# Kernel tuning notes

Hardware: AMD Instinct MI355X
Metric: run time of the kernel (lower is better)

Reference implementation:

```python
import jax, jax.numpy as jnp
import numpy as np

B, S, D = 4, 2048, 2048
H, KVH = 16, 8
HD = D // H          # 128
N_REP = H // KVH     # 2


def _rope(t, cos, sin):
    # t: [B,S,h,HD]; cos/sin: [S, HD//2]
    tr = t.reshape(*t.shape[:-1], HD // 2, 2)
    t0, t1 = tr[..., 0], tr[..., 1]
    c = cos[None, :, None, :]
    s = sin[None, :, None, :]
    o0 = t0 * c - t1 * s
    o1 = t0 * s + t1 * c
    return jnp.stack([o0, o1], axis=-1).reshape(t.shape)


def setup_inputs() -> dict:
    key = jax.random.key(0)
    ks = jax.random.split(key, 7)
    x = jax.random.normal(ks[0], (B, S, D), dtype=jnp.float32)
    wq = jax.random.normal(ks[1], (D, H * HD), dtype=jnp.float32) * 0.02
    wk = jax.random.normal(ks[2], (D, KVH * HD), dtype=jnp.float32) * 0.02
    wv = jax.random.normal(ks[3], (D, KVH * HD), dtype=jnp.float32) * 0.02
    wo = jax.random.normal(ks[4], (H * HD, D), dtype=jnp.float32) * 0.02
    # rotary angles as in precompute_pos_cis: theta=1e6-style base 10000
    freqs = 1.0 / (10000.0 ** (jnp.arange(0, HD, 2, dtype=jnp.float32) / HD))
    ang = jnp.outer(jnp.arange(S, dtype=jnp.float32), freqs)  # [S, HD//2]
    return {"x": x, "wq": wq, "wk": wk, "wv": wv, "wo": wo,
            "pos_cos": jnp.cos(ang), "pos_sin": jnp.sin(ang)}


def reference(x, wq, wk, wv, wo, pos_cos, pos_sin):
    q = (x @ wq).reshape(B, S, H, HD)
    k = (x @ wk).reshape(B, S, KVH, HD)
    v = (x @ wv).reshape(B, S, KVH, HD)
    q = _rope(q, pos_cos, pos_sin)
    k = _rope(k, pos_cos, pos_sin)
    # GQA repeat_kv: [B,S,KVH,HD] -> [B,S,H,HD]
    k = jnp.repeat(k, N_REP, axis=2)
    v = jnp.repeat(v, N_REP, axis=2)
    scale = 1.0 / jnp.sqrt(jnp.float32(HD))
    scores = jnp.einsum('bqhd,bkhd->bhqk', q, k) * scale
    causal = jnp.tril(jnp.ones((S, S), dtype=bool))
    scores = jnp.where(causal[None, None], scores, jnp.float32(-jnp.inf))
    attn = jax.nn.softmax(scores, axis=-1)
    out = jnp.einsum('bhqk,bkhd->bqhd', attn, v).reshape(B, S, H * HD)
    return out @ wo
```

## Files before the change

kernel.cpp:

```cpp
#include <hip/hip_runtime.h>
#include <stdint.h>

#define SEQ   2048
#define DIM   2048
#define NH    16
#define NKVH  8
#define HDIM  128
#define MTOT  8192
#define LOG2E 1.44269504088896340736f

typedef short bf16x8 __attribute__((ext_vector_type(8)));
typedef float f32x4  __attribute__((ext_vector_type(4)));
typedef unsigned short us4 __attribute__((ext_vector_type(4)));

#define MFMA(a, b, c) __builtin_amdgcn_mfma_f32_16x16x32_bf16((a), (b), (c), 0, 0, 0)

__device__ inline unsigned short f2bf(float f) {
    unsigned u = __builtin_bit_cast(unsigned, f);
    u = (u + 0x7FFFu + ((u >> 16) & 1u)) >> 16;
    return (unsigned short)u;
}

__device__ inline void stage16(const void* g, void* l) {
    __builtin_amdgcn_global_load_lds(
        (const __attribute__((address_space(1))) void*)g,
        (__attribute__((address_space(3))) void*)l,
        16, 0, 0);
}

__global__ void conv_x(const float* __restrict__ x, unsigned short* __restrict__ xb) {
    long i = ((long)blockIdx.x * 256 + threadIdx.x) * 4;
    float4 v = *(const float4*)(x + i);
    us4 o = { f2bf(v.x), f2bf(v.y), f2bf(v.z), f2bf(v.w) };
    *(us4*)(xb + i) = o;
}

__global__ void transpose_w(const float* __restrict__ in, unsigned short* __restrict__ out,
                            int N, int row_off) {
    __shared__ float t[32][33];
    int tx = threadIdx.x, ty = threadIdx.y;
    int n0 = blockIdx.x * 32, k0 = blockIdx.y * 32;
    for (int i = 0; i < 4; i++)
        t[ty + i * 8][tx] = in[(long)(k0 + ty + i * 8) * N + n0 + tx];
    __syncthreads();
    for (int i = 0; i < 4; i++)
        out[(long)(row_off + n0 + ty + i * 8) * 2048 + k0 + tx] = f2bf(t[tx][ty + i * 8]);
}

__global__ void transpose_v(const unsigned short* __restrict__ v, unsigned short* __restrict__ vt) {
    __shared__ unsigned short t[32][33];
    int tx = threadIdx.x, ty = threadIdx.y;
    int d0 = blockIdx.x * 32, s0 = blockIdx.y * 32, bk = blockIdx.z;
    const unsigned short* vin = v + (long)bk * SEQ * HDIM;
    unsigned short* vo = vt + (long)bk * HDIM * SEQ;
    for (int i = 0; i < 4; i++)
        t[ty + i * 8][tx] = vin[(long)(s0 + ty + i * 8) * HDIM + d0 + tx];
    __syncthreads();
    for (int i = 0; i < 4; i++)
        vo[(long)(d0 + ty + i * 8) * SEQ + s0 + tx] = t[tx][ty + i * 8];
}

__launch_bounds__(256, 2)
__global__ void qkv_gemm(const unsigned short* __restrict__ xb,
                         const unsigned short* __restrict__ wt,
                         const float* __restrict__ pcos, const float* __restrict__ psin,
                         unsigned short* __restrict__ qb, unsigned short* __restrict__ kbuf,
                         unsigned short* __restrict__ vbuf) {
    constexpr int K = DIM;
    __shared__ __align__(16) unsigned short As[128 * 64];
    __shared__ __align__(16) unsigned short Bs[128 * 64];
    const int tid = threadIdx.x;
    const int m0 = blockIdx.y * 128;
    const int n0 = blockIdx.x * 128;
    const int w = tid >> 6, lane = tid & 63, qq = lane >> 4, ln = lane & 15;
    const int wm = w >> 1, wn = w & 1;

    f32x4 acc[4][4] = {};

    const int arow = tid >> 3;
    const int aswz = ((tid & 7) ^ (arow & 7)) * 8;
    const unsigned short* ag = xb + (long)(m0 + arow) * K + aswz;
    const unsigned short* bg = wt + (long)(n0 + arow) * K + aswz;
    unsigned short* al = As + tid * 8;
    unsigned short* bl = Bs + tid * 8;

    for (int kk = 0; kk < K; kk += 64) {
        __syncthreads();
        stage16(ag + kk,          al);
        stage16(ag + kk + 32 * K, al + 2048);
        stage16(ag + kk + 64 * K, al + 4096);
        stage16(ag + kk + 96 * K, al + 6144);
        stage16(bg + kk,          bl);
        stage16(bg + kk + 32 * K, bl + 2048);
        stage16(bg + kk + 64 * K, bl + 4096);
        stage16(bg + kk + 96 * K, bl + 6144);
        __syncthreads();
        bf16x8 a[2][4], b[2][4];
        for (int ks = 0; ks < 2; ks++) {
            for (int mt = 0; mt < 4; mt++)
                a[ks][mt] = *(const bf16x8*)&As[(wm * 64 + mt * 16 + ln) * 64 + (((ks * 4 + qq) ^ (ln & 7)) * 8)];
            for (int nt = 0; nt < 4; nt++)
                b[ks][nt] = *(const bf16x8*)&Bs[(wn * 64 + nt * 16 + ln) * 64 + (((ks * 4 + qq) ^ (ln & 7)) * 8)];
        }
        for (int ks = 0; ks < 2; ks++)
            for (int mt = 0; mt < 4; mt++)
                for (int nt = 0; nt < 4; nt++)
                    acc[mt][nt] = MFMA(b[ks][nt], a[ks][mt], acc[mt][nt]);
    }

    const bool isv = (n0 >= 3072);
    for (int mt = 0; mt < 4; mt++) {
        int m = m0 + wm * 64 + mt * 16 + ln;
        int b_ = m >> 11, s = m & (SEQ - 1);
        const float* crow = pcos + s * 64;
        const float* srow = psin + s * 64;
        for (int nt = 0; nt < 4; nt++) {
            int n = n0 + wn * 64 + nt * 16 + qq * 4;
            int d = n & (HDIM - 1);
            f32x4 v = acc[mt][nt];
            float o0, o1, o2, o3;
            if (!isv) {
                int i = d >> 1;
                float2 cc = *(const float2*)(crow + i);
                float2 ss = *(const float2*)(srow + i);
                o0 = v[0] * cc.x - v[1] * ss.x;
                o1 = v[0] * ss.x + v[1] * cc.x;
                o2 = v[2] * cc.y - v[3] * ss.y;
                o3 = v[2] * ss.y + v[3] * cc.y;
            } else {
                o0 = v[0]; o1 = v[1]; o2 = v[2]; o3 = v[3];
            }
            us4 pu = { f2bf(o0), f2bf(o1), f2bf(o2), f2bf(o3) };
            if (n < 2048) {
                int hh = n >> 7;
                *(us4*)&qb[((long)(b_ * NH + hh) * SEQ + s) * HDIM + d] = pu;
            } else if (n < 3072) {
                int kvh = (n - 2048) >> 7;
                *(us4*)&kbuf[((long)(b_ * NKVH + kvh) * SEQ + s) * HDIM + d] = pu;
            } else {
                int kvh = (n - 3072) >> 7;
                *(us4*)&vbuf[((long)(b_ * NKVH + kvh) * SEQ + s) * HDIM + d] = pu;
            }
        }
    }
}

__launch_bounds__(256, 2)
__global__ void flash(const unsigned short* __restrict__ qb,
                      const unsigned short* __restrict__ kb,
                      const unsigned short* __restrict__ vtb,
                      unsigned short* __restrict__ aout) {
    __shared__ __align__(16) unsigned short KV[32768];
    const int tid = threadIdx.x;
    const int w = tid >> 6, lane = tid & 63, qq = lane >> 4, ln = lane & 15;
    unsigned short* Pseg = KV + w * 4096;

    int f = blockIdx.x + (blockIdx.y << 3) + (blockIdx.z << 7);
    int xcd = f & 7, j = f >> 3;
    int bkv = xcd + 8 * (j & 3);
    int b = bkv >> 3, kv = bkv & 7;
    int rem = j >> 2;
    int h = kv * 2 + (rem & 1);
    int qpair = rem >> 1;

    const unsigned short* qbase = qb + (long)(b * NH + h) * SEQ * HDIM;
    const unsigned short* kbase = kb + (long)(b * NKVH + kv) * SEQ * HDIM;
    const unsigned short* vbase = vtb + (long)(b * NKVH + kv) * HDIM * SEQ;
    const float SCL2 = 0.088388347648318447f * LOG2E;

    const int srow = tid >> 4;
    const int sswz = (tid & 15) ^ srow;

    for (int phase = 0; phase < 2; phase++) {
        const int qt = (phase == 0) ? qpair : 15 - qpair;
        const int q0 = qt * 128 + w * 32;

        bf16x8 qf[2][4];
        for (int nt = 0; nt < 2; nt++)
            for (int ks = 0; ks < 4; ks++)
                qf[nt][ks] = *(const bf16x8*)&qbase[(long)(q0 + nt * 16 + ln) * HDIM + ks * 32 + qq * 8];

        float m[2] = { -3e38f, -3e38f }, l[2] = { 0.f, 0.f };
        f32x4 oacc[8][2] = {};

        #pragma unroll 1
        for (int kt = 0; kt <= qt; kt++) {
            const int k0 = kt * 128;

            __syncthreads();
            char* kl = (char*)KV;
            #pragma unroll
            for (int r = 0; r < 8; r++) {
                int key = r * 16 + srow;
                stage16(kbase + (long)(k0 + key) * HDIM + sswz * 8, kl + r * 4096 + tid * 16);
            }
            #pragma unroll
            for (int r = 0; r < 8; r++) {
                int hd = r * 16 + srow;
                stage16(vbase + (long)hd * SEQ + k0 + sswz * 8, kl + 32768 + r * 4096 + tid * 16);
            }
            __syncthreads();

            f32x4 sacc[8][2] = {};
            #pragma unroll
            for (int mt = 0; mt < 8; mt++) {
                const unsigned short* kr = &KV[(mt * 16 + ln) * 128];
                bf16x8 kf0 = *(const bf16x8*)&kr[((0 + qq) ^ ln) * 8];
                bf16x8 kf1 = *(const bf16x8*)&kr[((4 + qq) ^ ln) * 8];
                bf16x8 kf2 = *(const bf16x8*)&kr[((8 + qq) ^ ln) * 8];
                bf16x8 kf3 = *(const bf16x8*)&kr[((12 + qq) ^ ln) * 8];
                sacc[mt][0] = MFMA(kf0, qf[0][0], sacc[mt][0]);
                sacc[mt][1] = MFMA(kf0, qf[1][0], sacc[mt][1]);
                sacc[mt][0] = MFMA(kf1, qf[0][1], sacc[mt][0]);
                sacc[mt][1] = MFMA(kf1, qf[1][1], sacc[mt][1]);
                sacc[mt][0] = MFMA(kf2, qf[0][2], sacc[mt][0]);
                sacc[mt][1] = MFMA(kf2, qf[1][2], sacc[mt][1]);
                sacc[mt][0] = MFMA(kf3, qf[0][3], sacc[mt][0]);
                sacc[mt][1] = MFMA(kf3, qf[1][3], sacc[mt][1]);
            }

            __syncthreads();

            const bool diag = (kt == qt);
            #pragma unroll
            for (int nt = 0; nt < 2; nt++) {
                const int q = q0 + nt * 16 + ln;
                float mx = m[nt];
                #pragma unroll
                for (int mt = 0; mt < 8; mt++)
                    #pragma unroll
                    for (int r = 0; r < 4; r++) {
                        float v = sacc[mt][nt][r];
                        if (diag && (k0 + mt * 16 + qq * 4 + r > q)) v = -3e38f;
                        sacc[mt][nt][r] = v;
                        mx = fmaxf(mx, v);
                    }
                mx = fmaxf(mx, __shfl_xor(mx, 16));
                mx = fmaxf(mx, __shfl_xor(mx, 32));
                float alpha = exp2f((m[nt] - mx) * SCL2);
                m[nt] = mx;
                float rs = 0.f;
                #pragma unroll
                for (int mt = 0; mt < 8; mt++) {
                    float p0 = exp2f((sacc[mt][nt][0] - mx) * SCL2);
                    float p1 = exp2f((sacc[mt][nt][1] - mx) * SCL2);
                    float p2 = exp2f((sacc[mt][nt][2] - mx) * SCL2);
                    float p3 = exp2f((sacc[mt][nt][3] - mx) * SCL2);
                    rs += (p0 + p1) + (p2 + p3);
                    us4 pu = { f2bf(p0), f2bf(p1), f2bf(p2), f2bf(p3) };
                    *(us4*)&Pseg[(nt * 16 + ln) * 128 + ((mt * 2 + (qq >> 1)) ^ ln) * 8 + (qq & 1) * 4] = pu;
                }
                rs += __shfl_xor(rs, 16);
                rs += __shfl_xor(rs, 32);
                l[nt] = l[nt] * alpha + rs;
                #pragma unroll
                for (int mt = 0; mt < 8; mt++)
                    #pragma unroll
                    for (int r = 0; r < 4; r++)
                        oacc[mt][nt][r] *= alpha;
            }

            bf16x8 pf[4][2];
            #pragma unroll
            for (int ks = 0; ks < 4; ks++)
                #pragma unroll
                for (int nt = 0; nt < 2; nt++)
                    pf[ks][nt] = *(const bf16x8*)&Pseg[(nt * 16 + ln) * 128 + ((ks * 4 + qq) ^ ln) * 8];
            #pragma unroll
            for (int mt = 0; mt < 8; mt++) {
                const unsigned short* vr = &KV[16384 + (mt * 16 + ln) * 128];
                bf16x8 vf0 = *(const bf16x8*)&vr[((0 + qq) ^ ln) * 8];
                bf16x8 vf1 = *(const bf16x8*)&vr[((4 + qq) ^ ln) * 8];
                bf16x8 vf2 = *(const bf16x8*)&vr[((8 + qq) ^ ln) * 8];
                bf16x8 vf3 = *(const bf16x8*)&vr[((12 + qq) ^ ln) * 8];
                oacc[mt][0] = MFMA(vf0, pf[0][0], oacc[mt][0]);
                oacc[mt][1] = MFMA(vf0, pf[0][1], oacc[mt][1]);
                oacc[mt][0] = MFMA(vf1, pf[1][0], oacc[mt][0]);
                oacc[mt][1] = MFMA(vf1, pf[1][1], oacc[mt][1]);
                oacc[mt][0] = MFMA(vf2, pf[2][0], oacc[mt][0]);
                oacc[mt][1] = MFMA(vf2, pf[2][1], oacc[mt][1]);
                oacc[mt][0] = MFMA(vf3, pf[3][0], oacc[mt][0]);
                oacc[mt][1] = MFMA(vf3, pf[3][1], oacc[mt][1]);
            }
        }

        #pragma unroll
        for (int nt = 0; nt < 2; nt++) {
            const int q = q0 + nt * 16 + ln;
            float inv = 1.f / l[nt];
            unsigned short* ao = aout + ((long)b * SEQ + q) * DIM + h * HDIM;
            #pragma unroll
            for (int mt = 0; mt < 8; mt++) {
                us4 o = { f2bf(oacc[mt][nt][0] * inv), f2bf(oacc[mt][nt][1] * inv),
                          f2bf(oacc[mt][nt][2] * inv), f2bf(oacc[mt][nt][3] * inv) };
                *(us4*)&ao[mt * 16 + qq * 4] = o;
            }
        }
    }
}

__launch_bounds__(256, 2)
__global__ void out_gemm(const unsigned short* __restrict__ ab,
                         const unsigned short* __restrict__ wt,
                         float* __restrict__ out) {
    constexpr int K = DIM;
    __shared__ __align__(16) unsigned short As[128 * 64];
    __shared__ __align__(16) unsigned short Bs[128 * 64];
    const int tid = threadIdx.x;
    const int m0 = blockIdx.y * 128;
    const int n0 = blockIdx.x * 128;
    const int w = tid >> 6, lane = tid & 63, qq = lane >> 4, ln = lane & 15;
    const int wm = w >> 1, wn = w & 1;

    f32x4 acc[4][4] = {};

    const int arow = tid >> 3;
    const int aswz = ((tid & 7) ^ (arow & 7)) * 8;
    const unsigned short* ag = ab + (long)(m0 + arow) * K + aswz;
    const unsigned short* bg = wt + (long)(n0 + arow) * K + aswz;
    unsigned short* al = As + tid * 8;
    unsigned short* bl = Bs + tid * 8;

    for (int kk = 0; kk < K; kk += 64) {
        __syncthreads();
        stage16(ag + kk,          al);
        stage16(ag + kk + 32 * K, al + 2048);
        stage16(ag + kk + 64 * K, al + 4096);
        stage16(ag + kk + 96 * K, al + 6144);
        stage16(bg + kk,          bl);
        stage16(bg + kk + 32 * K, bl + 2048);
        stage16(bg + kk + 64 * K, bl + 4096);
        stage16(bg + kk + 96 * K, bl + 6144);
        __syncthreads();
        bf16x8 a[2][4], b[2][4];
        for (int ks = 0; ks < 2; ks++) {
            for (int mt = 0; mt < 4; mt++)
                a[ks][mt] = *(const bf16x8*)&As[(wm * 64 + mt * 16 + ln) * 64 + (((ks * 4 + qq) ^ (ln & 7)) * 8)];
            for (int nt = 0; nt < 4; nt++)
                b[ks][nt] = *(const bf16x8*)&Bs[(wn * 64 + nt * 16 + ln) * 64 + (((ks * 4 + qq) ^ (ln & 7)) * 8)];
        }
        for (int ks = 0; ks < 2; ks++)
            for (int mt = 0; mt < 4; mt++)
                for (int nt = 0; nt < 4; nt++)
                    acc[mt][nt] = MFMA(a[ks][mt], b[ks][nt], acc[mt][nt]);
    }

    for (int mt = 0; mt < 4; mt++)
        for (int nt = 0; nt < 4; nt++) {
            int n = n0 + wn * 64 + nt * 16 + ln;
            for (int r = 0; r < 4; r++) {
                int m = m0 + wm * 64 + mt * 16 + qq * 4 + r;
                out[(long)m * DIM + n] = acc[mt][nt][r];
            }
        }
}

extern "C" void kernel_launch(void* const* d_in, const int* in_sizes, int n_in,
                              void* d_out, int out_size, void* d_ws, size_t ws_size,
                              hipStream_t stream) {
    const float* x    = (const float*)d_in[0];
    const float* wq   = (const float*)d_in[1];
    const float* wk   = (const float*)d_in[2];
    const float* wv   = (const float*)d_in[3];
    const float* wo   = (const float*)d_in[4];
    const float* pcos = (const float*)d_in[5];
    const float* psin = (const float*)d_in[6];
    float* out = (float*)d_out;

    char* ws = (char*)d_ws;
    unsigned short* xb    = (unsigned short*)(ws);
    unsigned short* wqkvt = (unsigned short*)(ws + 33554432L);
    unsigned short* wot   = (unsigned short*)(ws + 50331648L);
    unsigned short* qbuf  = (unsigned short*)(ws + 58720256L);
    unsigned short* kbuf  = (unsigned short*)(ws + 92274688L);
    unsigned short* vbuf  = (unsigned short*)(ws + 109051904L);
    unsigned short* vtb   = (unsigned short*)(ws + 125829120L);
    unsigned short* aout  = (unsigned short*)(ws + 142606336L);

    conv_x<<<16384, 256, 0, stream>>>(x, xb);
    transpose_w<<<dim3(64, 64), dim3(32, 8), 0, stream>>>(wq, wqkvt, 2048, 0);
    transpose_w<<<dim3(32, 64), dim3(32, 8), 0, stream>>>(wk, wqkvt, 1024, 2048);
    transpose_w<<<dim3(32, 64), dim3(32, 8), 0, stream>>>(wv, wqkvt, 1024, 3072);
    transpose_w<<<dim3(64, 64), dim3(32, 8), 0, stream>>>(wo, wot, 2048, 0);

    qkv_gemm<<<dim3(32, 64), 256, 0, stream>>>(xb, wqkvt, pcos, psin, qbuf, kbuf, vbuf);
    transpose_v<<<dim3(4, 64, 32), dim3(32, 8), 0, stream>>>(vbuf, vtb);
    flash<<<dim3(8, 16, 4), 256, 0, stream>>>(qbuf, kbuf, vtb, aout);
    out_gemm<<<dim3(16, 64), 256, 0, stream>>>(aout, wot, out);
}
```

Measured before the change: 548.4 us.

## Triple-buffer LDS and use 256x128 tiles with 512 threads in GEMMs

Both projection GEMMs move to 512-thread blocks computing 256x128 tiles, and the LDS staging becomes a three-stage ring. Global-to-LDS loads for tile t+2 are issued while MFMAs run on tile t, with explicit vmcnt waits, split barriers and setprio raised around the MFMA bursts. The aim is to hide global load latency and halve the per-iteration full barriers. In exchange it uses about 144KB of LDS per block, which limits occupancy, and relies on hand-placed waitcnt counts being correct.

```diff
diff --git a/kernel.cpp b/kernel.cpp
--- a/kernel.cpp
+++ b/kernel.cpp
@@ -60,17 +60,17 @@
         vo[(long)(d0 + ty + i * 8) * SEQ + s0 + tx] = t[tx][ty + i * 8];
 }
 
-__launch_bounds__(256, 2)
+__launch_bounds__(512, 2)
 __global__ void qkv_gemm(const unsigned short* __restrict__ xb,
                          const unsigned short* __restrict__ wt,
                          const float* __restrict__ pcos, const float* __restrict__ psin,
                          unsigned short* __restrict__ qb, unsigned short* __restrict__ kbuf,
                          unsigned short* __restrict__ vbuf) {
-    constexpr int K = DIM;
-    __shared__ __align__(16) unsigned short As[128 * 64];
-    __shared__ __align__(16) unsigned short Bs[128 * 64];
+    constexpr int K  = DIM;
+    constexpr int NT = K / 64;
+    __shared__ __align__(16) unsigned short sh[3 * 24576];
     const int tid = threadIdx.x;
-    const int m0 = blockIdx.y * 128;
+    const int m0 = blockIdx.y * 256;
     const int n0 = blockIdx.x * 128;
     const int w = tid >> 6, lane = tid & 63, qq = lane >> 4, ln = lane & 15;
     const int wm = w >> 1, wn = w & 1;
@@ -81,31 +81,79 @@
     const int aswz = ((tid & 7) ^ (arow & 7)) * 8;
     const unsigned short* ag = xb + (long)(m0 + arow) * K + aswz;
     const unsigned short* bg = wt + (long)(n0 + arow) * K + aswz;
-    unsigned short* al = As + tid * 8;
-    unsigned short* bl = Bs + tid * 8;
-
-    for (int kk = 0; kk < K; kk += 64) {
-        __syncthreads();
-        stage16(ag + kk,          al);
-        stage16(ag + kk + 32 * K, al + 2048);
-        stage16(ag + kk + 64 * K, al + 4096);
-        stage16(ag + kk + 96 * K, al + 6144);
-        stage16(bg + kk,          bl);
-        stage16(bg + kk + 32 * K, bl + 2048);
-        stage16(bg + kk + 64 * K, bl + 4096);
-        stage16(bg + kk + 96 * K, bl + 6144);
-        __syncthreads();
-        bf16x8 a[2][4], b[2][4];
-        for (int ks = 0; ks < 2; ks++) {
-            for (int mt = 0; mt < 4; mt++)
-                a[ks][mt] = *(const bf16x8*)&As[(wm * 64 + mt * 16 + ln) * 64 + (((ks * 4 + qq) ^ (ln & 7)) * 8)];
+
+    #pragma unroll
+    for (int t = 0; t < 2; t++) {
+        unsigned short* sa = sh + t * 24576 + tid * 8;
+        unsigned short* sb = sa + 16384;
+        const unsigned short* agk = ag + t * 64;
+        const unsigned short* bgk = bg + t * 64;
+        stage16(agk,            sa);
+        stage16(agk + 64  * K,  sa + 4096);
+        stage16(agk + 128 * K,  sa + 8192);
+        stage16(agk + 192 * K,  sa + 12288);
+        stage16(bgk,            sb);
+        stage16(bgk + 64  * K,  sb + 4096);
+    }
+
+    int cur = 0, stg = 2;
+    #pragma unroll 1
+    for (int t = 0; t < NT; t++) {
+        if (t == NT - 1) asm volatile("s_waitcnt vmcnt(0) lgkmcnt(0)" ::: "memory");
+        else             asm volatile("s_waitcnt vmcnt(6) lgkmcnt(0)" ::: "memory");
+        asm volatile("s_barrier" ::: "memory");
+
+        const unsigned short* Ab = sh + cur * 24576;
+        const unsigned short* Bb = Ab + 16384;
+        unsigned short* sa = sh + stg * 24576 + tid * 8;
+        unsigned short* sb = sa + 16384;
+        const unsigned short* agk = ag + (t + 2) * 64;
+        const unsigned short* bgk = bg + (t + 2) * 64;
+        const bool doStage = (t + 2 < NT);
+
+        bf16x8 a0[4], b0[4];
+        #pragma unroll
+        for (int mt = 0; mt < 4; mt++)
+            a0[mt] = *(const bf16x8*)&Ab[(wm * 64 + mt * 16 + ln) * 64 + ((qq ^ (ln & 7)) * 8)];
+        #pragma unroll
+        for (int nt = 0; nt < 4; nt++)
+            b0[nt] = *(const bf16x8*)&Bb[(wn * 64 + nt * 16 + ln) * 64 + ((qq ^ (ln & 7)) * 8)];
+        if (doStage) {
+            stage16(agk,           sa);
+            stage16(agk + 64 * K,  sa + 4096);
+            stage16(agk + 128 * K, sa + 8192);
+        }
+        __builtin_amdgcn_s_setprio(1);
+        #pragma unroll
+        for (int mt = 0; mt < 4; mt++)
+            #pragma unroll
             for (int nt = 0; nt < 4; nt++)
-                b[ks][nt] = *(const bf16x8*)&Bs[(wn * 64 + nt * 16 + ln) * 64 + (((ks * 4 + qq) ^ (ln & 7)) * 8)];
-        }
-        for (int ks = 0; ks < 2; ks++)
-            for (int mt = 0; mt < 4; mt++)
-                for (int nt = 0; nt < 4; nt++)
-                    acc[mt][nt] = MFMA(b[ks][nt], a[ks][mt], acc[mt][nt]);
+                acc[mt][nt] = MFMA(b0[nt], a0[mt], acc[mt][nt]);
+        __builtin_amdgcn_s_setprio(0);
+        __builtin_amdgcn_s_barrier();
+
+        bf16x8 a1[4], b1[4];
+        #pragma unroll
+        for (int mt = 0; mt < 4; mt++)
+            a1[mt] = *(const bf16x8*)&Ab[(wm * 64 + mt * 16 + ln) * 64 + (((4 + qq) ^ (ln & 7)) * 8)];
+        #pragma unroll
+        for (int nt = 0; nt < 4; nt++)
+            b1[nt] = *(const bf16x8*)&Bb[(wn * 64 + nt * 16 + ln) * 64 + (((4 + qq) ^ (ln & 7)) * 8)];
+        if (doStage) {
+            stage16(agk + 192 * K, sa + 12288);
+            stage16(bgk,           sb);
+            stage16(bgk + 64 * K,  sb + 4096);
+        }
+        __builtin_amdgcn_s_setprio(1);
+        #pragma unroll
+        for (int mt = 0; mt < 4; mt++)
+            #pragma unroll
+            for (int nt = 0; nt < 4; nt++)
+                acc[mt][nt] = MFMA(b1[nt], a1[mt], acc[mt][nt]);
+        __builtin_amdgcn_s_setprio(0);
+
+        cur = (cur == 2) ? 0 : cur + 1;
+        stg = (stg == 2) ? 0 : stg + 1;
     }
 
     const bool isv = (n0 >= 3072);
@@ -299,15 +347,15 @@
     }
 }
 
-__launch_bounds__(256, 2)
+__launch_bounds__(512, 2)
 __global__ void out_gemm(const unsigned short* __restrict__ ab,
                          const unsigned short* __restrict__ wt,
                          float* __restrict__ out) {
-    constexpr int K = DIM;
-    __shared__ __align__(16) unsigned short As[128 * 64];
-    __shared__ __align__(16) unsigned short Bs[128 * 64];
+    constexpr int K  = DIM;
+    constexpr int NT = K / 64;
+    __shared__ __align__(16) unsigned short sh[3 * 24576];
     const int tid = threadIdx.x;
-    const int m0 = blockIdx.y * 128;
+    const int m0 = blockIdx.y * 256;
     const int n0 = blockIdx.x * 128;
     const int w = tid >> 6, lane = tid & 63, qq = lane >> 4, ln = lane & 15;
     const int wm = w >> 1, wn = w & 1;
@@ -318,31 +366,79 @@
     const int aswz = ((tid & 7) ^ (arow & 7)) * 8;
     const unsigned short* ag = ab + (long)(m0 + arow) * K + aswz;
     const unsigned short* bg = wt + (long)(n0 + arow) * K + aswz;
-    unsigned short* al = As + tid * 8;
-    unsigned short* bl = Bs + tid * 8;
-
-    for (int kk = 0; kk < K; kk += 64) {
-        __syncthreads();
-        stage16(ag + kk,          al);
-        stage16(ag + kk + 32 * K, al + 2048);
-        stage16(ag + kk + 64 * K, al + 4096);
-        stage16(ag + kk + 96 * K, al + 6144);
-        stage16(bg + kk,          bl);
-        stage16(bg + kk + 32 * K, bl + 2048);
-        stage16(bg + kk + 64 * K, bl + 4096);
-        stage16(bg + kk + 96 * K, bl + 6144);
-        __syncthreads();
-        bf16x8 a[2][4], b[2][4];
-        for (int ks = 0; ks < 2; ks++) {
-            for (int mt = 0; mt < 4; mt++)
-                a[ks][mt] = *(const bf16x8*)&As[(wm * 64 + mt * 16 + ln) * 64 + (((ks * 4 + qq) ^ (ln & 7)) * 8)];
+
+    #pragma unroll
+    for (int t = 0; t < 2; t++) {
+        unsigned short* sa = sh + t * 24576 + tid * 8;
+        unsigned short* sb = sa + 16384;
+        const unsigned short* agk = ag + t * 64;
+        const unsigned short* bgk = bg + t * 64;
+        stage16(agk,            sa);
+        stage16(agk + 64  * K,  sa + 4096);
+        stage16(agk + 128 * K,  sa + 8192);
+        stage16(agk + 192 * K,  sa + 12288);
+        stage16(bgk,            sb);
+        stage16(bgk + 64  * K,  sb + 4096);
+    }
+
+    int cur = 0, stg = 2;
+    #pragma unroll 1
+    for (int t = 0; t < NT; t++) {
+        if (t == NT - 1) asm volatile("s_waitcnt vmcnt(0) lgkmcnt(0)" ::: "memory");
+        else             asm volatile("s_waitcnt vmcnt(6) lgkmcnt(0)" ::: "memory");
+        asm volatile("s_barrier" ::: "memory");
+
+        const unsigned short* Ab = sh + cur * 24576;
+        const unsigned short* Bb = Ab + 16384;
+        unsigned short* sa = sh + stg * 24576 + tid * 8;
+        unsigned short* sb = sa + 16384;
+        const unsigned short* agk = ag + (t + 2) * 64;
+        const unsigned short* bgk = bg + (t + 2) * 64;
+        const bool doStage = (t + 2 < NT);
+
+        bf16x8 a0[4], b0[4];
+        #pragma unroll
+        for (int mt = 0; mt < 4; mt++)
+            a0[mt] = *(const bf16x8*)&Ab[(wm * 64 + mt * 16 + ln) * 64 + ((qq ^ (ln & 7)) * 8)];
+        #pragma unroll
+        for (int nt = 0; nt < 4; nt++)
+            b0[nt] = *(const bf16x8*)&Bb[(wn * 64 + nt * 16 + ln) * 64 + ((qq ^ (ln & 7)) * 8)];
+        if (doStage) {
+            stage16(agk,           sa);
+            stage16(agk + 64 * K,  sa + 4096);
+            stage16(agk + 128 * K, sa + 8192);
+        }
+        __builtin_amdgcn_s_setprio(1);
+        #pragma unroll
+        for (int mt = 0; mt < 4; mt++)
+            #pragma unroll
             for (int nt = 0; nt < 4; nt++)
-                b[ks][nt] = *(const bf16x8*)&Bs[(wn * 64 + nt * 16 + ln) * 64 + (((ks * 4 + qq) ^ (ln & 7)) * 8)];
-        }
-        for (int ks = 0; ks < 2; ks++)
-            for (int mt = 0; mt < 4; mt++)
-                for (int nt = 0; nt < 4; nt++)
-                    acc[mt][nt] = MFMA(a[ks][mt], b[ks][nt], acc[mt][nt]);
+                acc[mt][nt] = MFMA(a0[mt], b0[nt], acc[mt][nt]);
+        __builtin_amdgcn_s_setprio(0);
+        __builtin_amdgcn_s_barrier();
+
+        bf16x8 a1[4], b1[4];
+        #pragma unroll
+        for (int mt = 0; mt < 4; mt++)
+            a1[mt] = *(const bf16x8*)&Ab[(wm * 64 + mt * 16 + ln) * 64 + (((4 + qq) ^ (ln & 7)) * 8)];
+        #pragma unroll
+        for (int nt = 0; nt < 4; nt++)
+            b1[nt] = *(const bf16x8*)&Bb[(wn * 64 + nt * 16 + ln) * 64 + (((4 + qq) ^ (ln & 7)) * 8)];
+        if (doStage) {
+            stage16(agk + 192 * K, sa + 12288);
+            stage16(bgk,           sb);
+            stage16(bgk + 64 * K,  sb + 4096);
+        }
+        __builtin_amdgcn_s_setprio(1);
+        #pragma unroll
+        for (int mt = 0; mt < 4; mt++)
+            #pragma unroll
+            for (int nt = 0; nt < 4; nt++)
+                acc[mt][nt] = MFMA(a1[mt], b1[nt], acc[mt][nt]);
+        __builtin_amdgcn_s_setprio(0);
+
+        cur = (cur == 2) ? 0 : cur + 1;
+        stg = (stg == 2) ? 0 : stg + 1;
     }
 
     for (int mt = 0; mt < 4; mt++)
@@ -383,8 +479,8 @@
     transpose_w<<<dim3(32, 64), dim3(32, 8), 0, stream>>>(wv, wqkvt, 1024, 3072);
     transpose_w<<<dim3(64, 64), dim3(32, 8), 0, stream>>>(wo, wot, 2048, 0);
 
-    qkv_gemm<<<dim3(32, 64), 256, 0, stream>>>(xb, wqkvt, pcos, psin, qbuf, kbuf, vbuf);
+    qkv_gemm<<<dim3(32, 32), 512, 0, stream>>>(xb, wqkvt, pcos, psin, qbuf, kbuf, vbuf);
     transpose_v<<<dim3(4, 64, 32), dim3(32, 8), 0, stream>>>(vbuf, vtb);
     flash<<<dim3(8, 16, 4), 256, 0, stream>>>(qbuf, kbuf, vtb, aout);
-    out_gemm<<<dim3(16, 64), 256, 0, stream>>>(aout, wot, out);
-}
+    out_gemm<<<dim3(16, 32), 512, 0, stream>>>(aout, wot, out);
+}
```

Result: faster. 520.7 us (-5.0%).

## Rewrite projection GEMMs as 256x256 tiles with double-buffered LDS pipelining

Applied to the files above, without the earlier changes.

Both the QKV and output projection GEMMs go from 128x128 tiles with 256 threads to 256x256 tiles with 512 threads (8 waves, each computing 128x64). The K loop is now software-pipelined over two 64 KB LDS buffers: global-to-LDS loads for later k-steps are issued in quarters between four MFMA phases, with explicit vmcnt/lgkmcnt waits, raw s_barrier and s_setprio. The aim is to hide global load latency behind MFMA work and to raise arithmetic intensity per byte staged. In exchange, accumulator register pressure is higher, the LDS footprint larger, and the grid has fewer blocks, which can limit occupancy.

```diff
diff --git a/kernel.cpp b/kernel.cpp
--- a/kernel.cpp
+++ b/kernel.cpp
@@ -60,64 +60,135 @@
         vo[(long)(d0 + ty + i * 8) * SEQ + s0 + tx] = t[tx][ty + i * 8];
 }
 
-__launch_bounds__(256, 2)
+
+#define STAGEH(p_, op_, h_, t_) do {                                              \
+    unsigned short* d_ = sh + (p_) * 32768 + (op_) * 16384 + (h_) * 8192 + tid * 8; \
+    const unsigned short* s_ = ((op_) ? bg : ag) + (long)((h_) * 128) * K + (t_) * 64; \
+    stage16(s_, d_); stage16(s_ + 64 * K, d_ + 4096); } while (0)
+
+#define BARRIER() asm volatile("s_barrier" ::: "memory")
+#define WAITLGKM() asm volatile("s_waitcnt lgkmcnt(0)" ::: "memory")
+
+__launch_bounds__(512, 2)
 __global__ void qkv_gemm(const unsigned short* __restrict__ xb,
                          const unsigned short* __restrict__ wt,
                          const float* __restrict__ pcos, const float* __restrict__ psin,
                          unsigned short* __restrict__ qb, unsigned short* __restrict__ kbuf,
                          unsigned short* __restrict__ vbuf) {
-    constexpr int K = DIM;
-    __shared__ __align__(16) unsigned short As[128 * 64];
-    __shared__ __align__(16) unsigned short Bs[128 * 64];
+    constexpr int K  = DIM;
+    constexpr int NT = K / 64;
+    __shared__ __align__(16) unsigned short sh[65536];
     const int tid = threadIdx.x;
-    const int m0 = blockIdx.y * 128;
-    const int n0 = blockIdx.x * 128;
+    const int m0 = blockIdx.y * 256;
+    const int n0 = blockIdx.x * 256;
     const int w = tid >> 6, lane = tid & 63, qq = lane >> 4, ln = lane & 15;
-    const int wm = w >> 1, wn = w & 1;
-
-    f32x4 acc[4][4] = {};
-
-    const int arow = tid >> 3;
-    const int aswz = ((tid & 7) ^ (arow & 7)) * 8;
-    const unsigned short* ag = xb + (long)(m0 + arow) * K + aswz;
-    const unsigned short* bg = wt + (long)(n0 + arow) * K + aswz;
-    unsigned short* al = As + tid * 8;
-    unsigned short* bl = Bs + tid * 8;
-
-    for (int kk = 0; kk < K; kk += 64) {
-        __syncthreads();
-        stage16(ag + kk,          al);
-        stage16(ag + kk + 32 * K, al + 2048);
-        stage16(ag + kk + 64 * K, al + 4096);
-        stage16(ag + kk + 96 * K, al + 6144);
-        stage16(bg + kk,          bl);
-        stage16(bg + kk + 32 * K, bl + 2048);
-        stage16(bg + kk + 64 * K, bl + 4096);
-        stage16(bg + kk + 96 * K, bl + 6144);
-        __syncthreads();
-        bf16x8 a[2][4], b[2][4];
-        for (int ks = 0; ks < 2; ks++) {
-            for (int mt = 0; mt < 4; mt++)
-                a[ks][mt] = *(const bf16x8*)&As[(wm * 64 + mt * 16 + ln) * 64 + (((ks * 4 + qq) ^ (ln & 7)) * 8)];
-            for (int nt = 0; nt < 4; nt++)
-                b[ks][nt] = *(const bf16x8*)&Bs[(wn * 64 + nt * 16 + ln) * 64 + (((ks * 4 + qq) ^ (ln & 7)) * 8)];
-        }
-        for (int ks = 0; ks < 2; ks++)
-            for (int mt = 0; mt < 4; mt++)
-                for (int nt = 0; nt < 4; nt++)
-                    acc[mt][nt] = MFMA(b[ks][nt], a[ks][mt], acc[mt][nt]);
+    const int wm = w >> 2, wn = w & 3;
+
+    f32x4 acc[8][4] = {};
+
+    const int rowq = tid >> 3;
+    const int cswz = ((tid & 7) ^ (rowq & 7)) * 8;
+    const unsigned short* ag = xb + (long)(m0 + rowq) * K + cswz;
+    const unsigned short* bg = wt + (long)(n0 + rowq) * K + cswz;
+
+    const int aoff = wm * 8192 + ln * 64;
+    const int boff = 16384 + (wn >> 1) * 8192 + ((wn & 1) * 64 + ln) * 64;
+    const int swz0 = ((0 + qq) ^ (ln & 7)) * 8;
+    const int swz1 = ((4 + qq) ^ (ln & 7)) * 8;
+
+    STAGEH(0, 1, 0, 0); STAGEH(0, 1, 1, 0); STAGEH(0, 0, 0, 0); STAGEH(0, 0, 1, 0);
+    STAGEH(1, 1, 0, 1); STAGEH(1, 0, 0, 1); STAGEH(1, 0, 1, 1);
+
+    #pragma unroll 1
+    for (int t = 0; t < NT; t++) {
+        const int p = t & 1, pn = p ^ 1;
+        if (t >= NT - 1) asm volatile("s_waitcnt vmcnt(0)" ::: "memory");
+        else             asm volatile("s_waitcnt vmcnt(6)" ::: "memory");
+        BARRIER();
+
+        const unsigned short* Ab = sh + p * 32768;
+        bf16x8 af[8][2], bf_[4][2];
+
+        #pragma unroll
+        for (int fc = 0; fc < 4; fc++) {
+            bf_[fc][0] = *(const bf16x8*)&Ab[boff + fc * 1024 + swz0];
+            bf_[fc][1] = *(const bf16x8*)&Ab[boff + fc * 1024 + swz1];
+        }
+        #pragma unroll
+        for (int fr = 0; fr < 4; fr++) {
+            af[fr][0] = *(const bf16x8*)&Ab[aoff + fr * 1024 + swz0];
+            af[fr][1] = *(const bf16x8*)&Ab[aoff + fr * 1024 + swz1];
+        }
+        if (t + 1 < NT) STAGEH(pn, 1, 1, t + 1);
+        BARRIER();
+        WAITLGKM();
+        __builtin_amdgcn_s_setprio(1);
+        #pragma unroll
+        for (int fr = 0; fr < 4; fr++)
+            #pragma unroll
+            for (int fc = 0; fc < 2; fc++) {
+                acc[fr][fc] = MFMA(bf_[fc][0], af[fr][0], acc[fr][fc]);
+                acc[fr][fc] = MFMA(bf_[fc][1], af[fr][1], acc[fr][fc]);
+            }
+        __builtin_amdgcn_s_setprio(0);
+        BARRIER();
+
+        #pragma unroll
+        for (int fr = 4; fr < 8; fr++) {
+            af[fr][0] = *(const bf16x8*)&Ab[aoff + fr * 1024 + swz0];
+            af[fr][1] = *(const bf16x8*)&Ab[aoff + fr * 1024 + swz1];
+        }
+        if (t + 2 < NT) STAGEH(p, 1, 0, t + 2);
+        BARRIER();
+        WAITLGKM();
+        __builtin_amdgcn_s_setprio(1);
+        #pragma unroll
+        for (int fr = 0; fr < 4; fr++)
+            #pragma unroll
+            for (int fc = 2; fc < 4; fc++) {
+                acc[fr][fc] = MFMA(bf_[fc][0], af[fr][0], acc[fr][fc]);
+                acc[fr][fc] = MFMA(bf_[fc][1], af[fr][1], acc[fr][fc]);
+            }
+        __builtin_amdgcn_s_setprio(0);
+        BARRIER();
+
+        if (t + 2 < NT) STAGEH(p, 0, 0, t + 2);
+        BARRIER();
+        __builtin_amdgcn_s_setprio(1);
+        #pragma unroll
+        for (int fr = 4; fr < 8; fr++)
+            #pragma unroll
+            for (int fc = 0; fc < 2; fc++) {
+                acc[fr][fc] = MFMA(bf_[fc][0], af[fr][0], acc[fr][fc]);
+                acc[fr][fc] = MFMA(bf_[fc][1], af[fr][1], acc[fr][fc]);
+            }
+        __builtin_amdgcn_s_setprio(0);
+        BARRIER();
+
+        if (t + 2 < NT) STAGEH(p, 0, 1, t + 2);
+        BARRIER();
+        __builtin_amdgcn_s_setprio(1);
+        #pragma unroll
+        for (int fr = 4; fr < 8; fr++)
+            #pragma unroll
+            for (int fc = 2; fc < 4; fc++) {
+                acc[fr][fc] = MFMA(bf_[fc][0], af[fr][0], acc[fr][fc]);
+                acc[fr][fc] = MFMA(bf_[fc][1], af[fr][1], acc[fr][fc]);
+            }
+        __builtin_amdgcn_s_setprio(0);
+        BARRIER();
     }
 
     const bool isv = (n0 >= 3072);
-    for (int mt = 0; mt < 4; mt++) {
-        int m = m0 + wm * 64 + mt * 16 + ln;
+    for (int fr = 0; fr < 8; fr++) {
+        int m = m0 + wm * 128 + fr * 16 + ln;
         int b_ = m >> 11, s = m & (SEQ - 1);
         const float* crow = pcos + s * 64;
         const float* srow = psin + s * 64;
-        for (int nt = 0; nt < 4; nt++) {
-            int n = n0 + wn * 64 + nt * 16 + qq * 4;
+        for (int fc = 0; fc < 4; fc++) {
+            int n = n0 + wn * 64 + fc * 16 + qq * 4;
             int d = n & (HDIM - 1);
-            f32x4 v = acc[mt][nt];
+            f32x4 v = acc[fr][fc];
             float o0, o1, o2, o3;
             if (!isv) {
                 int i = d >> 1;
@@ -299,58 +370,120 @@
     }
 }
 
-__launch_bounds__(256, 2)
+__launch_bounds__(512, 2)
 __global__ void out_gemm(const unsigned short* __restrict__ ab,
                          const unsigned short* __restrict__ wt,
                          float* __restrict__ out) {
-    constexpr int K = DIM;
-    __shared__ __align__(16) unsigned short As[128 * 64];
-    __shared__ __align__(16) unsigned short Bs[128 * 64];
+    constexpr int K  = DIM;
+    constexpr int NT = K / 64;
+    __shared__ __align__(16) unsigned short sh[65536];
     const int tid = threadIdx.x;
-    const int m0 = blockIdx.y * 128;
-    const int n0 = blockIdx.x * 128;
+    const int m0 = blockIdx.y * 256;
+    const int n0 = blockIdx.x * 256;
     const int w = tid >> 6, lane = tid & 63, qq = lane >> 4, ln = lane & 15;
-    const int wm = w >> 1, wn = w & 1;
-
-    f32x4 acc[4][4] = {};
-
-    const int arow = tid >> 3;
-    const int aswz = ((tid & 7) ^ (arow & 7)) * 8;
-    const unsigned short* ag = ab + (long)(m0 + arow) * K + aswz;
-    const unsigned short* bg = wt + (long)(n0 + arow) * K + aswz;
-    unsigned short* al = As + tid * 8;
-    unsigned short* bl = Bs + tid * 8;
-
-    for (int kk = 0; kk < K; kk += 64) {
-        __syncthreads();
-        stage16(ag + kk,          al);
-        stage16(ag + kk + 32 * K, al + 2048);
-        stage16(ag + kk + 64 * K, al + 4096);
-        stage16(ag + kk + 96 * K, al + 6144);
-        stage16(bg + kk,          bl);
-        stage16(bg + kk + 32 * K, bl + 2048);
-        stage16(bg + kk + 64 * K, bl + 4096);
-        stage16(bg + kk + 96 * K, bl + 6144);
-        __syncthreads();
-        bf16x8 a[2][4], b[2][4];
-        for (int ks = 0; ks < 2; ks++) {
-            for (int mt = 0; mt < 4; mt++)
-                a[ks][mt] = *(const bf16x8*)&As[(wm * 64 + mt * 16 + ln) * 64 + (((ks * 4 + qq) ^ (ln & 7)) * 8)];
-            for (int nt = 0; nt < 4; nt++)
-                b[ks][nt] = *(const bf16x8*)&Bs[(wn * 64 + nt * 16 + ln) * 64 + (((ks * 4 + qq) ^ (ln & 7)) * 8)];
-        }
-        for (int ks = 0; ks < 2; ks++)
-            for (int mt = 0; mt < 4; mt++)
-                for (int nt = 0; nt < 4; nt++)
-                    acc[mt][nt] = MFMA(a[ks][mt], b[ks][nt], acc[mt][nt]);
+    const int wm = w >> 2, wn = w & 3;
+
+    f32x4 acc[8][4] = {};
+
+    const int rowq = tid >> 3;
+    const int cswz = ((tid & 7) ^ (rowq & 7)) * 8;
+    const unsigned short* ag = ab + (long)(m0 + rowq) * K + cswz;
+    const unsigned short* bg = wt + (long)(n0 + rowq) * K + cswz;
+
+    const int aoff = wm * 8192 + ln * 64;
+    const int boff = 16384 + (wn >> 1) * 8192 + ((wn & 1) * 64 + ln) * 64;
+    const int swz0 = ((0 + qq) ^ (ln & 7)) * 8;
+    const int swz1 = ((4 + qq) ^ (ln & 7)) * 8;
+
+    STAGEH(0, 1, 0, 0); STAGEH(0, 1, 1, 0); STAGEH(0, 0, 0, 0); STAGEH(0, 0, 1, 0);
+    STAGEH(1, 1, 0, 1); STAGEH(1, 0, 0, 1); STAGEH(1, 0, 1, 1);
+
+    #pragma unroll 1
+    for (int t = 0; t < NT; t++) {
+        const int p = t & 1, pn = p ^ 1;
+        if (t >= NT - 1) asm volatile("s_waitcnt vmcnt(0)" ::: "memory");
+        else             asm volatile("s_waitcnt vmcnt(6)" ::: "memory");
+        BARRIER();
+
+        const unsigned short* Ab = sh + p * 32768;
+        bf16x8 af[8][2], bf_[4][2];
+
+        #pragma unroll
+        for (int fc = 0; fc < 4; fc++) {
+            bf_[fc][0] = *(const bf16x8*)&Ab[boff + fc * 1024 + swz0];
+            bf_[fc][1] = *(const bf16x8*)&Ab[boff + fc * 1024 + swz1];
+        }
+        #pragma unroll
+        for (int fr = 0; fr < 4; fr++) {
+            af[fr][0] = *(const bf16x8*)&Ab[aoff + fr * 1024 + swz0];
+            af[fr][1] = *(const bf16x8*)&Ab[aoff + fr * 1024 + swz1];
+        }
+        if (t + 1 < NT) STAGEH(pn, 1, 1, t + 1);
+        BARRIER();
+        WAITLGKM();
+        __builtin_amdgcn_s_setprio(1);
+        #pragma unroll
+        for (int fr = 0; fr < 4; fr++)
+            #pragma unroll
+            for (int fc = 0; fc < 2; fc++) {
+                acc[fr][fc] = MFMA(af[fr][0], bf_[fc][0], acc[fr][fc]);
+                acc[fr][fc] = MFMA(af[fr][1], bf_[fc][1], acc[fr][fc]);
+            }
+        __builtin_amdgcn_s_setprio(0);
+        BARRIER();
+
+        #pragma unroll
+        for (int fr = 4; fr < 8; fr++) {
+            af[fr][0] = *(const bf16x8*)&Ab[aoff + fr * 1024 + swz0];
+            af[fr][1] = *(const bf16x8*)&Ab[aoff + fr * 1024 + swz1];
+        }
+        if (t + 2 < NT) STAGEH(p, 1, 0, t + 2);
+        BARRIER();
+        WAITLGKM();
+        __builtin_amdgcn_s_setprio(1);
+        #pragma unroll
+        for (int fr = 0; fr < 4; fr++)
+            #pragma unroll
+            for (int fc = 2; fc < 4; fc++) {
+                acc[fr][fc] = MFMA(af[fr][0], bf_[fc][0], acc[fr][fc]);
+                acc[fr][fc] = MFMA(af[fr][1], bf_[fc][1], acc[fr][fc]);
+            }
+        __builtin_amdgcn_s_setprio(0);
+        BARRIER();
+
+        if (t + 2 < NT) STAGEH(p, 0, 0, t + 2);
+        BARRIER();
+        __builtin_amdgcn_s_setprio(1);
+        #pragma unroll
+        for (int fr = 4; fr < 8; fr++)
+            #pragma unroll
+            for (int fc = 0; fc < 2; fc++) {
+                acc[fr][fc] = MFMA(af[fr][0], bf_[fc][0], acc[fr][fc]);
+                acc[fr][fc] = MFMA(af[fr][1], bf_[fc][1], acc[fr][fc]);
+            }
+        __builtin_amdgcn_s_setprio(0);
+        BARRIER();
+
+        if (t + 2 < NT) STAGEH(p, 0, 1, t + 2);
+        BARRIER();
+        __builtin_amdgcn_s_setprio(1);
+        #pragma unroll
+        for (int fr = 4; fr < 8; fr++)
+            #pragma unroll
+            for (int fc = 2; fc < 4; fc++) {
+                acc[fr][fc] = MFMA(af[fr][0], bf_[fc][0], acc[fr][fc]);
+                acc[fr][fc] = MFMA(af[fr][1], bf_[fc][1], acc[fr][fc]);
+            }
+        __builtin_amdgcn_s_setprio(0);
+        BARRIER();
     }
 
-    for (int mt = 0; mt < 4; mt++)
-        for (int nt = 0; nt < 4; nt++) {
-            int n = n0 + wn * 64 + nt * 16 + ln;
+    for (int fr = 0; fr < 8; fr++)
+        for (int fc = 0; fc < 4; fc++) {
+            int n = n0 + wn * 64 + fc * 16 + ln;
             for (int r = 0; r < 4; r++) {
-                int m = m0 + wm * 64 + mt * 16 + qq * 4 + r;
-                out[(long)m * DIM + n] = acc[mt][nt][r];
+                int m = m0 + wm * 128 + fr * 16 + qq * 4 + r;
+                out[(long)m * DIM + n] = acc[fr][fc][r];
             }
         }
 }
@@ -383,8 +516,8 @@
     transpose_w<<<dim3(32, 64), dim3(32, 8), 0, stream>>>(wv, wqkvt, 1024, 3072);
     transpose_w<<<dim3(64, 64), dim3(32, 8), 0, stream>>>(wo, wot, 2048, 0);
 
-    qkv_gemm<<<dim3(32, 64), 256, 0, stream>>>(xb, wqkvt, pcos, psin, qbuf, kbuf, vbuf);
+    qkv_gemm<<<dim3(16, 32), 512, 0, stream>>>(xb, wqkvt, pcos, psin, qbuf, kbuf, vbuf);
     transpose_v<<<dim3(4, 64, 32), dim3(32, 8), 0, stream>>>(vbuf, vtb);
     flash<<<dim3(8, 16, 4), 256, 0, stream>>>(qbuf, kbuf, vtb, aout);
-    out_gemm<<<dim3(16, 64), 256, 0, stream>>>(aout, wot, out);
-}
+    out_gemm<<<dim3(8, 32), 512, 0, stream>>>(aout, wot, out);
+}
```

Result: faster. 512.1 us (-6.6%).
